# Kernel tuning notes

Hardware: AMD Instinct MI355X
Metric: run time of the kernel (lower is better)

## Reference

```python
import jax, jax.numpy as jnp
import numpy as np

TEMPERATURE = 0.1
NUM_RISK_GROUPS = 4
SIM_WEIGHT = 1.0
CONTRAST_WEIGHT = 0.1
NEG = jnp.float32(-1e9)  # finite stand-in for -inf (grad-safe, exp() == 0 in fp32)


def setup_inputs() -> dict:
    key = jax.random.key(0)
    k1, k2, k3, k4 = jax.random.split(key, 4)
    N, D = 8192, 256
    return {
        "log_risks": jax.random.normal(k1, (N,), dtype=jnp.float32),
        "times": jax.random.uniform(k2, (N,), dtype=jnp.float32),
        "censor": jnp.ones((N,), dtype=jnp.int32),
        "wsi_embeddings": jax.random.normal(k3, (N, D), dtype=jnp.float32),
        "omic_embeddings": jax.random.normal(k4, (N, D), dtype=jnp.float32),
    }


def _cox_loss(log_risks, times, censor):
    lr = jnp.clip(log_risks, -10.0, 10.0)
    order = jnp.argsort(-times)  # descending times
    slr = lr[order]
    sc = censor[order]
    # at-risk sum for index i is sum_{j<=i} exp(slr_j) (arange <= i mask) -> cumsum
    at_risk = jnp.cumsum(jnp.exp(slr))
    li = slr - jnp.log(at_risk + 1e-15)
    mask = (sc == 1)
    cnt = jnp.maximum(jnp.sum(mask), 1)
    return -jnp.sum(jnp.where(mask, li, 0.0)) / cnt


def _similarity_loss(a, b):
    na = jnp.maximum(jnp.linalg.norm(a, axis=1), 1e-8)
    nb = jnp.maximum(jnp.linalg.norm(b, axis=1), 1e-8)
    cos = jnp.clip(jnp.sum(a * b, axis=1) / (na * nb), -1.0, 1.0)
    return jnp.mean(1.0 - cos)


def _contrastive_loss(emb, times):
    # NOTE: assumes censor == 1 for all samples (as in setup_inputs), so the
    # uncensored subset is the whole batch and shapes stay static.
    G = NUM_RISK_GROUPS
    q = jnp.quantile(times, jnp.linspace(0.0, 1.0, G + 1))
    # group = #thresholds q[1..G] that t >= ; max bucket clipped to G-1
    groups = jnp.clip(jnp.sum(times[:, None] >= q[None, 1:], axis=1), 0, G - 1)
    z = emb / jnp.maximum(jnp.linalg.norm(emb, axis=1, keepdims=True), 1e-12)
    sim = (z @ z.T) / TEMPERATURE  # [N, N]
    N = emb.shape[0]
    eye = jnp.eye(N, dtype=bool)
    same = groups[:, None] == groups[None, :]
    pos = same & ~eye
    offdiag = ~eye  # pos | neg == all off-diagonal entries
    lse_pos = jax.nn.logsumexp(jnp.where(pos, sim, NEG), axis=1)
    lse_all = jax.nn.logsumexp(jnp.where(offdiag, sim, NEG), axis=1)
    neg_any = jnp.any(~same & ~eye, axis=1)
    valid = jnp.any(pos, axis=1) & neg_any
    loss = -lse_pos + lse_all
    cnt = jnp.maximum(jnp.sum(valid), 1)
    return jnp.sum(jnp.where(valid, loss, 0.0)) / cnt


def reference(log_risks, times, censor, wsi_embeddings, omic_embeddings):
    cox = _cox_loss(log_risks, times, censor)
    sim = _similarity_loss(wsi_embeddings, omic_embeddings)
    c_wsi = _contrastive_loss(wsi_embeddings, times)
    c_omic = _contrastive_loss(omic_embeddings, times)
    contrast = (c_wsi + c_omic) / 2.0
    return cox + SIM_WEIGHT * sim + CONTRAST_WEIGHT * contrast
```

## Files before the change

kernel.cpp:

```cpp
#include <hip/hip_runtime.h>


#define NN 8192
#define DD 256
#define NSLOT 64

typedef __attribute__((ext_vector_type(4))) float f32x4;
typedef __attribute__((ext_vector_type(4))) int i32x4;
typedef __attribute__((ext_vector_type(2))) long l64x2;

__device__ inline void gl_lds16(const void* g, void* l) {
  __builtin_amdgcn_global_load_lds(
      (const __attribute__((address_space(1))) unsigned int*)g,
      (__attribute__((address_space(3))) unsigned int*)l, 16, 0, 0);
}

__global__ void __launch_bounds__(256) k_rank_atrisk(
    const float* __restrict__ times, const float* __restrict__ lr,
    int* __restrict__ rank, float* __restrict__ at_risk) {
  __shared__ __align__(16) float st[512];
  __shared__ __align__(16) float se[512];
  const int tid = threadIdx.x;
  const int i = blockIdx.x * 256 + tid;
  const int jbase = blockIdx.y * 512;
  for (int p = tid; p < 512; p += 256) {
    float t = times[jbase + p];
    float l = lr[jbase + p];
    l = fminf(fmaxf(l, -10.f), 10.f);
    st[p] = t;
    se[p] = __expf(l);
  }
  __syncthreads();
  const float ti = times[i];
  int rk = 0;
  float ar = 0.f;
  for (int p4 = 0; p4 < 512; p4 += 4) {
    float4 tv = *(const float4*)&st[p4];
    float4 ev = *(const float4*)&se[p4];
    const int j0 = jbase + p4;
#define K1_STEP(c, jo)                                              \
    {                                                               \
      bool c1 = (c < ti) || ((c == ti) && ((j0 + jo) < i));         \
      rk += c1 ? 1 : 0;                                             \
      ar += c1 ? 0.f : ((jo == 0) ? ev.x : (jo == 1) ? ev.y         \
                         : (jo == 2) ? ev.z : ev.w);                \
    }
    K1_STEP(tv.x, 0) K1_STEP(tv.y, 1) K1_STEP(tv.z, 2) K1_STEP(tv.w, 3)
#undef K1_STEP
  }
  atomicAdd(&rank[i], rk);
  atomicAdd(&at_risk[i], ar);
}

__global__ void __launch_bounds__(256) k_rows(
    const float* __restrict__ lr, const int* __restrict__ censor,
    const float* __restrict__ wsi, const float* __restrict__ omic,
    const int* __restrict__ rank, const float* __restrict__ at_risk,
    unsigned char* __restrict__ pw, unsigned char* __restrict__ po,
    float* __restrict__ slots) {
  __shared__ float red[4][3];
  const int tid = threadIdx.x;
  const int lane = tid & 63;
  const int wv = tid >> 6;
  const int i = blockIdx.x * 4 + wv;
  const float4 w = ((const float4*)(wsi + (size_t)i * DD))[lane];
  const float4 o = ((const float4*)(omic + (size_t)i * DD))[lane];
  float nw = w.x * w.x + w.y * w.y + w.z * w.z + w.w * w.w;
  float no = o.x * o.x + o.y * o.y + o.z * o.z + o.w * o.w;
  float dd = w.x * o.x + w.y * o.y + w.z * o.z + w.w * o.w;
  for (int m = 1; m < 64; m <<= 1) {
    nw += __shfl_xor(nw, m);
    no += __shfl_xor(no, m);
    dd += __shfl_xor(dd, m);
  }
  const float nws = sqrtf(nw), nos = sqrtf(no);
  if (lane == 0) {
    float c = dd / (fmaxf(nws, 1e-8f) * fmaxf(nos, 1e-8f));
    c = fminf(fmaxf(c, -1.f), 1.f);
    float l = fminf(fmaxf(lr[i], -10.f), 10.f);
    float li = l - logf(at_risk[i] + 1e-15f);
    bool cen = (censor[i] == 1);
    red[wv][0] = cen ? li : 0.f;
    red[wv][1] = cen ? 1.f : 0.f;
    red[wv][2] = 1.f - c;
  }
  const int r = rank[i];
  const float iw = 1.f / fmaxf(nws, 1e-12f);
  const float io = 1.f / fmaxf(nos, 1e-12f);
  int zw = __builtin_amdgcn_cvt_pk_fp8_f32(w.x * iw, w.y * iw, 0, false);
  zw = __builtin_amdgcn_cvt_pk_fp8_f32(w.z * iw, w.w * iw, zw, true);
  int zo = __builtin_amdgcn_cvt_pk_fp8_f32(o.x * io, o.y * io, 0, false);
  zo = __builtin_amdgcn_cvt_pk_fp8_f32(o.z * io, o.w * io, zo, true);
  const size_t off = ((size_t)((lane >> 4) * 4 + ((lane >> 1) & 3)) * NN + r) * 16
                     + ((lane >> 3) & 1) * 8 + (lane & 1) * 4;
  *(unsigned int*)(pw + off) = (unsigned int)zw;
  *(unsigned int*)(po + off) = (unsigned int)zo;
  __syncthreads();
  if (tid < 3) {
    float v = red[0][tid] + red[1][tid] + red[2][tid] + red[3][tid];
    atomicAdd(&slots[tid * NSLOT + (blockIdx.x & (NSLOT - 1))], v);
  }
}

__global__ void __launch_bounds__(256, 3) k_contrast(
    const unsigned char* __restrict__ pw, const unsigned char* __restrict__ po,
    float* __restrict__ gsum) {
  __shared__ __align__(16) unsigned char sbuf[2][16384];
  const int tid = threadIdx.x;
  const int lane = tid & 63;
  const int wv = tid >> 6;
  const int lo = lane & 15, q = lane >> 4;
  const int cb = blockIdx.x, rb = blockIdx.y, mz = blockIdx.z;
  const unsigned char* __restrict__ pk = (mz == 0) ? pw : po;
  const int rowbase = rb * 256 + wv * 64;
  const int colstart = cb * 512;
  const int g = cb >> 2;

  i32x4 afrag[4][4];
#pragma unroll
  for (int rt = 0; rt < 4; ++rt) {
    const size_t row = rowbase + rt * 16 + lo;
#pragma unroll
    for (int kp = 0; kp < 4; ++kp)
      afrag[rt][kp] = *(const i32x4*)(pk + ((size_t)(kp * 4 + q) * NN + row) * 16);
  }

  const unsigned char* gsrc[4];
#pragma unroll
  for (int p = 0; p < 4; ++p) {
    const int u = (wv * 4 + p) * 64 + lane;
    gsrc[p] = pk + ((size_t)(((u >> 6) & 3) * 4 + ((u >> 4) & 3)) * NN
                    + colstart + (u >> 8) * 16 + (u & 15)) * 16;
  }
  unsigned char* const ldb = &sbuf[0][(size_t)wv * 4096];

#pragma unroll
  for (int p = 0; p < 4; ++p) gl_lds16(gsrc[p], ldb + p * 1024);
  __syncthreads();

  float s[4][4] = {{0.f}};

#pragma unroll 1
  for (int st = 0; st < 8; ++st) {
    if (st < 7) {
      const size_t adv = (size_t)(st + 1) * 1024;
      const size_t bofs = ((st + 1) & 1) ? 16384 : 0;
#pragma unroll
      for (int p = 0; p < 4; ++p) gl_lds16(gsrc[p] + adv, ldb + bofs + p * 1024);
    }
    const unsigned char* buf = &sbuf[st & 1][0];
    const bool diagw = (rowbase == colstart + st * 64);
#pragma unroll
    for (int ct = 0; ct < 4; ++ct) {
      f32x4 acc[4];
#pragma unroll
      for (int rt = 0; rt < 4; ++rt) { f32x4 z = {0.f, 0.f, 0.f, 0.f}; acc[rt] = z; }
#pragma unroll
      for (int kh = 0; kh < 2; ++kh) {
        l64x2 b0 = __builtin_bit_cast(l64x2,
            *(const i32x4*)&buf[(ct * 4 + kh * 2 + 0) * 1024 + lane * 16]);
        l64x2 b1 = __builtin_bit_cast(l64x2,
            *(const i32x4*)&buf[(ct * 4 + kh * 2 + 1) * 1024 + lane * 16]);
#pragma unroll
        for (int rt = 0; rt < 4; ++rt) {
          l64x2 a0 = __builtin_bit_cast(l64x2, afrag[rt][kh * 2 + 0]);
          acc[rt] = __builtin_amdgcn_mfma_f32_16x16x32_fp8_fp8(a0[0], b0[0], acc[rt], 0, 0, 0);
          acc[rt] = __builtin_amdgcn_mfma_f32_16x16x32_fp8_fp8(a0[1], b0[1], acc[rt], 0, 0, 0);
        }
#pragma unroll
        for (int rt = 0; rt < 4; ++rt) {
          l64x2 a1 = __builtin_bit_cast(l64x2, afrag[rt][kh * 2 + 1]);
          acc[rt] = __builtin_amdgcn_mfma_f32_16x16x32_fp8_fp8(a1[0], b1[0], acc[rt], 0, 0, 0);
          acc[rt] = __builtin_amdgcn_mfma_f32_16x16x32_fp8_fp8(a1[1], b1[1], acc[rt], 0, 0, 0);
        }
      }
      if (diagw) {
#pragma unroll
        for (int rt = 0; rt < 4; ++rt)
#pragma unroll
          for (int r = 0; r < 4; ++r) {
            float e = __expf(fmaf(acc[rt][r], 10.f, -10.f));
            if (rt == ct && lo == q * 4 + r) e = 0.f;
            s[rt][r] += e;
          }
      } else {
#pragma unroll
        for (int rt = 0; rt < 4; ++rt)
#pragma unroll
          for (int r = 0; r < 4; ++r)
            s[rt][r] += __expf(fmaf(acc[rt][r], 10.f, -10.f));
      }
    }
    __syncthreads();
  }

#pragma unroll
  for (int rt = 0; rt < 4; ++rt)
#pragma unroll
    for (int r = 0; r < 4; ++r) {
      float v = s[rt][r];
      v += __shfl_xor(v, 1); v += __shfl_xor(v, 2);
      v += __shfl_xor(v, 4); v += __shfl_xor(v, 8);
      if (lo == 0) {
        const int row = rowbase + rt * 16 + q * 4 + r;
        atomicAdd(&gsum[((size_t)mz * NN + row) * 4 + g], v);
      }
    }
}

__global__ void __launch_bounds__(256) k_lse(
    const float* __restrict__ gsum, float* __restrict__ slots) {
  __shared__ float r4[4];
  const int tid = threadIdx.x;
  const int lane = tid & 63, wv = tid >> 6;
  const int idx = blockIdx.x * 256 + tid;
  const float4 v = ((const float4*)gsum)[idx];
  const int row = idx & (NN - 1);
  const int gg = row >> 11;
  const float sg = (gg == 0) ? v.x : (gg == 1) ? v.y : (gg == 2) ? v.z : v.w;
  float loss = logf(v.x + v.y + v.z + v.w) - logf(sg);
  for (int m = 1; m < 64; m <<= 1) loss += __shfl_xor(loss, m);
  if (lane == 0) r4[wv] = loss;
  __syncthreads();
  if (tid == 0)
    atomicAdd(&slots[3 * NSLOT + (blockIdx.x & (NSLOT - 1))],
              r4[0] + r4[1] + r4[2] + r4[3]);
}

__global__ void k_final(const float* __restrict__ slots, float* __restrict__ out) {
  const int lane = threadIdx.x & 63;
  float cox_s = (lane < NSLOT) ? slots[0 * NSLOT + lane] : 0.f;
  float cnt_s = (lane < NSLOT) ? slots[1 * NSLOT + lane] : 0.f;
  float sim_s = (lane < NSLOT) ? slots[2 * NSLOT + lane] : 0.f;
  float con_s = (lane < NSLOT) ? slots[3 * NSLOT + lane] : 0.f;
  for (int m = 1; m < 64; m <<= 1) {
    cox_s += __shfl_xor(cox_s, m);
    cnt_s += __shfl_xor(cnt_s, m);
    sim_s += __shfl_xor(sim_s, m);
    con_s += __shfl_xor(con_s, m);
  }
  if (lane == 0) {
    float cnt = fmaxf(cnt_s, 1.f);
    float cox = -cox_s / cnt;
    float sim = sim_s / (float)NN;
    float contrast = 0.1f * 0.5f * con_s / (float)NN;
    out[0] = cox + sim + contrast;
  }
}

extern "C" void kernel_launch(void* const* d_in, const int* in_sizes, int n_in,
                              void* d_out, int out_size, void* d_ws, size_t ws_size,
                              hipStream_t stream) {
  const float* lr = (const float*)d_in[0];
  const float* times = (const float*)d_in[1];
  const int* censor = (const int*)d_in[2];
  const float* wsi = (const float*)d_in[3];
  const float* omic = (const float*)d_in[4];
  float* out = (float*)d_out;

  char* ws = (char*)d_ws;
  int* rank = (int*)ws;
  float* at_risk = (float*)(ws + 32768);
  float* slots = (float*)(ws + 65536);
  float* gsum = (float*)(ws + 66560);
  unsigned char* pw = (unsigned char*)(ws + 393216);
  unsigned char* po = (unsigned char*)(ws + 393216 + 2097152);

  (void)hipMemsetAsync(d_ws, 0, 328704, stream);
  k_rank_atrisk<<<dim3(32, 16), 256, 0, stream>>>(times, lr, rank, at_risk);
  k_rows<<<2048, 256, 0, stream>>>(lr, censor, wsi, omic, rank, at_risk, pw, po, slots);
  k_contrast<<<dim3(16, 32, 2), 256, 0, stream>>>(pw, po, gsum);
  k_lse<<<64, 256, 0, stream>>>(gsum, slots);
  k_final<<<1, 64, 0, stream>>>(slots, out);
}
```

Measured before the change: 169.7 us.

## Fuse rank/at-risk into row kernel, shrink contrast tiles, merge final reductions

Drops the separate rank/at-risk kernel and the memset. Each wave in k_rows now computes its row's rank and at-risk sum itself by scanning all times, and k_rows also zeroes gsum. k_contrast gives each wave 32 rows instead of 64, which doubles the grid and raises the occupancy hint, and the LSE and final reductions merge into one 1024-thread kernel. This cuts launches and atomics, but every wave now does an O(N) scan, which adds redundant loads and compute, and the single-block finale reduces 16K rows serially per thread.

```diff
diff --git a/kernel.cpp b/kernel.cpp
--- a/kernel.cpp
+++ b/kernel.cpp
@@ -3,7 +3,6 @@
 
 #define NN 8192
 #define DD 256
-#define NSLOT 64
 
 typedef __attribute__((ext_vector_type(4))) float f32x4;
 typedef __attribute__((ext_vector_type(4))) int i32x4;
@@ -15,54 +14,24 @@
       (__attribute__((address_space(3))) unsigned int*)l, 16, 0, 0);
 }
 
-__global__ void __launch_bounds__(256) k_rank_atrisk(
-    const float* __restrict__ times, const float* __restrict__ lr,
-    int* __restrict__ rank, float* __restrict__ at_risk) {
-  __shared__ __align__(16) float st[512];
-  __shared__ __align__(16) float se[512];
-  const int tid = threadIdx.x;
-  const int i = blockIdx.x * 256 + tid;
-  const int jbase = blockIdx.y * 512;
-  for (int p = tid; p < 512; p += 256) {
-    float t = times[jbase + p];
-    float l = lr[jbase + p];
-    l = fminf(fmaxf(l, -10.f), 10.f);
-    st[p] = t;
-    se[p] = __expf(l);
-  }
-  __syncthreads();
-  const float ti = times[i];
-  int rk = 0;
-  float ar = 0.f;
-  for (int p4 = 0; p4 < 512; p4 += 4) {
-    float4 tv = *(const float4*)&st[p4];
-    float4 ev = *(const float4*)&se[p4];
-    const int j0 = jbase + p4;
-#define K1_STEP(c, jo)                                              \
-    {                                                               \
-      bool c1 = (c < ti) || ((c == ti) && ((j0 + jo) < i));         \
-      rk += c1 ? 1 : 0;                                             \
-      ar += c1 ? 0.f : ((jo == 0) ? ev.x : (jo == 1) ? ev.y         \
-                         : (jo == 2) ? ev.z : ev.w);                \
-    }
-    K1_STEP(tv.x, 0) K1_STEP(tv.y, 1) K1_STEP(tv.z, 2) K1_STEP(tv.w, 3)
-#undef K1_STEP
-  }
-  atomicAdd(&rank[i], rk);
-  atomicAdd(&at_risk[i], ar);
-}
-
 __global__ void __launch_bounds__(256) k_rows(
-    const float* __restrict__ lr, const int* __restrict__ censor,
+    const float* __restrict__ lr, const float* __restrict__ times,
+    const int* __restrict__ censor,
     const float* __restrict__ wsi, const float* __restrict__ omic,
-    const int* __restrict__ rank, const float* __restrict__ at_risk,
     unsigned char* __restrict__ pw, unsigned char* __restrict__ po,
-    float* __restrict__ slots) {
+    float* __restrict__ pslots, float* __restrict__ gsum) {
+  __shared__ __align__(16) float st[1024];
+  __shared__ __align__(16) float se[1024];
   __shared__ float red[4][3];
   const int tid = threadIdx.x;
   const int lane = tid & 63;
   const int wv = tid >> 6;
   const int i = blockIdx.x * 4 + wv;
+
+  if (blockIdx.x < 64) {
+    ((f32x4*)gsum)[blockIdx.x * 256 + tid] = (f32x4){0.f, 0.f, 0.f, 0.f};
+  }
+
   const float4 w = ((const float4*)(wsi + (size_t)i * DD))[lane];
   const float4 o = ((const float4*)(omic + (size_t)i * DD))[lane];
   float nw = w.x * w.x + w.y * w.y + w.z * w.z + w.w * w.w;
@@ -74,17 +43,46 @@
     dd += __shfl_xor(dd, m);
   }
   const float nws = sqrtf(nw), nos = sqrtf(no);
+
+  const float ti = times[i];
+  int rk = 0;
+  float ar = 0.f;
+  for (int c = 0; c < 8; ++c) {
+    __syncthreads();
+    for (int p = tid; p < 1024; p += 256) {
+      float t = times[c * 1024 + p];
+      float l = lr[c * 1024 + p];
+      st[p] = t;
+      se[p] = __expf(fminf(fmaxf(l, -10.f), 10.f));
+    }
+    __syncthreads();
+#pragma unroll 4
+    for (int jt = 0; jt < 16; ++jt) {
+      const int p = jt * 64 + lane;
+      const float t = st[p];
+      const float e = se[p];
+      const bool c1 = (t < ti) || ((t == ti) && ((c * 1024 + p) < i));
+      rk += c1 ? 1 : 0;
+      ar += c1 ? 0.f : e;
+    }
+  }
+  for (int m = 1; m < 64; m <<= 1) {
+    rk += __shfl_xor(rk, m);
+    ar += __shfl_xor(ar, m);
+  }
+
   if (lane == 0) {
     float c = dd / (fmaxf(nws, 1e-8f) * fmaxf(nos, 1e-8f));
     c = fminf(fmaxf(c, -1.f), 1.f);
     float l = fminf(fmaxf(lr[i], -10.f), 10.f);
-    float li = l - logf(at_risk[i] + 1e-15f);
+    float li = l - logf(ar + 1e-15f);
     bool cen = (censor[i] == 1);
     red[wv][0] = cen ? li : 0.f;
     red[wv][1] = cen ? 1.f : 0.f;
     red[wv][2] = 1.f - c;
   }
-  const int r = rank[i];
+
+  const int r = rk;
   const float iw = 1.f / fmaxf(nws, 1e-12f);
   const float io = 1.f / fmaxf(nos, 1e-12f);
   int zw = __builtin_amdgcn_cvt_pk_fp8_f32(w.x * iw, w.y * iw, 0, false);
@@ -97,12 +95,12 @@
   *(unsigned int*)(po + off) = (unsigned int)zo;
   __syncthreads();
   if (tid < 3) {
-    float v = red[0][tid] + red[1][tid] + red[2][tid] + red[3][tid];
-    atomicAdd(&slots[tid * NSLOT + (blockIdx.x & (NSLOT - 1))], v);
-  }
-}
-
-__global__ void __launch_bounds__(256, 3) k_contrast(
+    pslots[blockIdx.x * 4 + tid] =
+        red[0][tid] + red[1][tid] + red[2][tid] + red[3][tid];
+  }
+}
+
+__global__ void __launch_bounds__(256, 4) k_contrast(
     const unsigned char* __restrict__ pw, const unsigned char* __restrict__ po,
     float* __restrict__ gsum) {
   __shared__ __align__(16) unsigned char sbuf[2][16384];
@@ -112,13 +110,13 @@
   const int lo = lane & 15, q = lane >> 4;
   const int cb = blockIdx.x, rb = blockIdx.y, mz = blockIdx.z;
   const unsigned char* __restrict__ pk = (mz == 0) ? pw : po;
-  const int rowbase = rb * 256 + wv * 64;
+  const int rowbase = rb * 128 + wv * 32;
   const int colstart = cb * 512;
   const int g = cb >> 2;
 
-  i32x4 afrag[4][4];
-#pragma unroll
-  for (int rt = 0; rt < 4; ++rt) {
+  i32x4 afrag[2][4];
+#pragma unroll
+  for (int rt = 0; rt < 2; ++rt) {
     const size_t row = rowbase + rt * 16 + lo;
 #pragma unroll
     for (int kp = 0; kp < 4; ++kp)
@@ -138,7 +136,8 @@
   for (int p = 0; p < 4; ++p) gl_lds16(gsrc[p], ldb + p * 1024);
   __syncthreads();
 
-  float s[4][4] = {{0.f}};
+  float s[2][4] = {{0.f}};
+  const int dctbase = (wv & 1) * 2;
 
 #pragma unroll 1
   for (int st = 0; st < 8; ++st) {
@@ -149,53 +148,52 @@
       for (int p = 0; p < 4; ++p) gl_lds16(gsrc[p] + adv, ldb + bofs + p * 1024);
     }
     const unsigned char* buf = &sbuf[st & 1][0];
-    const bool diagw = (rowbase == colstart + st * 64);
+    const bool diagw = ((rowbase >> 6) == ((colstart + st * 64) >> 6));
 #pragma unroll
     for (int ct = 0; ct < 4; ++ct) {
-      f32x4 acc[4];
-#pragma unroll
-      for (int rt = 0; rt < 4; ++rt) { f32x4 z = {0.f, 0.f, 0.f, 0.f}; acc[rt] = z; }
+      f32x4 a0 = {0.f, 0.f, 0.f, 0.f}, a1 = {0.f, 0.f, 0.f, 0.f};
 #pragma unroll
       for (int kh = 0; kh < 2; ++kh) {
         l64x2 b0 = __builtin_bit_cast(l64x2,
             *(const i32x4*)&buf[(ct * 4 + kh * 2 + 0) * 1024 + lane * 16]);
         l64x2 b1 = __builtin_bit_cast(l64x2,
             *(const i32x4*)&buf[(ct * 4 + kh * 2 + 1) * 1024 + lane * 16]);
-#pragma unroll
-        for (int rt = 0; rt < 4; ++rt) {
-          l64x2 a0 = __builtin_bit_cast(l64x2, afrag[rt][kh * 2 + 0]);
-          acc[rt] = __builtin_amdgcn_mfma_f32_16x16x32_fp8_fp8(a0[0], b0[0], acc[rt], 0, 0, 0);
-          acc[rt] = __builtin_amdgcn_mfma_f32_16x16x32_fp8_fp8(a0[1], b0[1], acc[rt], 0, 0, 0);
+        l64x2 x0 = __builtin_bit_cast(l64x2, afrag[0][kh * 2 + 0]);
+        l64x2 x1 = __builtin_bit_cast(l64x2, afrag[0][kh * 2 + 1]);
+        l64x2 y0 = __builtin_bit_cast(l64x2, afrag[1][kh * 2 + 0]);
+        l64x2 y1 = __builtin_bit_cast(l64x2, afrag[1][kh * 2 + 1]);
+        a0 = __builtin_amdgcn_mfma_f32_16x16x32_fp8_fp8(x0[0], b0[0], a0, 0, 0, 0);
+        a1 = __builtin_amdgcn_mfma_f32_16x16x32_fp8_fp8(y0[0], b0[0], a1, 0, 0, 0);
+        a0 = __builtin_amdgcn_mfma_f32_16x16x32_fp8_fp8(x0[1], b0[1], a0, 0, 0, 0);
+        a1 = __builtin_amdgcn_mfma_f32_16x16x32_fp8_fp8(y0[1], b0[1], a1, 0, 0, 0);
+        a0 = __builtin_amdgcn_mfma_f32_16x16x32_fp8_fp8(x1[0], b1[0], a0, 0, 0, 0);
+        a1 = __builtin_amdgcn_mfma_f32_16x16x32_fp8_fp8(y1[0], b1[0], a1, 0, 0, 0);
+        a0 = __builtin_amdgcn_mfma_f32_16x16x32_fp8_fp8(x1[1], b1[1], a0, 0, 0, 0);
+        a1 = __builtin_amdgcn_mfma_f32_16x16x32_fp8_fp8(y1[1], b1[1], a1, 0, 0, 0);
+      }
+      if (diagw) {
+#pragma unroll
+        for (int r = 0; r < 4; ++r) {
+          float e0 = __expf(fmaf(a0[r], 10.f, -10.f));
+          float e1 = __expf(fmaf(a1[r], 10.f, -10.f));
+          if (ct == dctbase + 0 && lo == q * 4 + r) e0 = 0.f;
+          if (ct == dctbase + 1 && lo == q * 4 + r) e1 = 0.f;
+          s[0][r] += e0;
+          s[1][r] += e1;
         }
-#pragma unroll
-        for (int rt = 0; rt < 4; ++rt) {
-          l64x2 a1 = __builtin_bit_cast(l64x2, afrag[rt][kh * 2 + 1]);
-          acc[rt] = __builtin_amdgcn_mfma_f32_16x16x32_fp8_fp8(a1[0], b1[0], acc[rt], 0, 0, 0);
-          acc[rt] = __builtin_amdgcn_mfma_f32_16x16x32_fp8_fp8(a1[1], b1[1], acc[rt], 0, 0, 0);
+      } else {
+#pragma unroll
+        for (int r = 0; r < 4; ++r) {
+          s[0][r] += __expf(fmaf(a0[r], 10.f, -10.f));
+          s[1][r] += __expf(fmaf(a1[r], 10.f, -10.f));
         }
       }
-      if (diagw) {
-#pragma unroll
-        for (int rt = 0; rt < 4; ++rt)
-#pragma unroll
-          for (int r = 0; r < 4; ++r) {
-            float e = __expf(fmaf(acc[rt][r], 10.f, -10.f));
-            if (rt == ct && lo == q * 4 + r) e = 0.f;
-            s[rt][r] += e;
-          }
-      } else {
-#pragma unroll
-        for (int rt = 0; rt < 4; ++rt)
-#pragma unroll
-          for (int r = 0; r < 4; ++r)
-            s[rt][r] += __expf(fmaf(acc[rt][r], 10.f, -10.f));
-      }
     }
     __syncthreads();
   }
 
 #pragma unroll
-  for (int rt = 0; rt < 4; ++rt)
+  for (int rt = 0; rt < 2; ++rt)
 #pragma unroll
     for (int r = 0; r < 4; ++r) {
       float v = s[rt][r];
@@ -208,43 +206,41 @@
     }
 }
 
-__global__ void __launch_bounds__(256) k_lse(
-    const float* __restrict__ gsum, float* __restrict__ slots) {
-  __shared__ float r4[4];
+__global__ void __launch_bounds__(1024) k_finale(
+    const float* __restrict__ pslots, const float* __restrict__ gsum,
+    float* __restrict__ out) {
+  __shared__ float rsum[16][4];
   const int tid = threadIdx.x;
   const int lane = tid & 63, wv = tid >> 6;
-  const int idx = blockIdx.x * 256 + tid;
-  const float4 v = ((const float4*)gsum)[idx];
-  const int row = idx & (NN - 1);
-  const int gg = row >> 11;
-  const float sg = (gg == 0) ? v.x : (gg == 1) ? v.y : (gg == 2) ? v.z : v.w;
-  float loss = logf(v.x + v.y + v.z + v.w) - logf(sg);
-  for (int m = 1; m < 64; m <<= 1) loss += __shfl_xor(loss, m);
-  if (lane == 0) r4[wv] = loss;
+  float cox = 0.f, cnt = 0.f, sim = 0.f, con = 0.f;
+  for (int b = tid; b < 2048; b += 1024) {
+    const float4 v = ((const float4*)pslots)[b];
+    cox += v.x; cnt += v.y; sim += v.z;
+  }
+  for (int idx = tid; idx < 2 * NN; idx += 1024) {
+    const float4 v = ((const float4*)gsum)[idx];
+    const int row = idx & (NN - 1);
+    const int gg = row >> 11;
+    const float sg = (gg == 0) ? v.x : (gg == 1) ? v.y : (gg == 2) ? v.z : v.w;
+    con += logf(v.x + v.y + v.z + v.w) - logf(sg);
+  }
+  for (int m = 1; m < 64; m <<= 1) {
+    cox += __shfl_xor(cox, m);
+    cnt += __shfl_xor(cnt, m);
+    sim += __shfl_xor(sim, m);
+    con += __shfl_xor(con, m);
+  }
+  if (lane == 0) {
+    rsum[wv][0] = cox; rsum[wv][1] = cnt; rsum[wv][2] = sim; rsum[wv][3] = con;
+  }
   __syncthreads();
-  if (tid == 0)
-    atomicAdd(&slots[3 * NSLOT + (blockIdx.x & (NSLOT - 1))],
-              r4[0] + r4[1] + r4[2] + r4[3]);
-}
-
-__global__ void k_final(const float* __restrict__ slots, float* __restrict__ out) {
-  const int lane = threadIdx.x & 63;
-  float cox_s = (lane < NSLOT) ? slots[0 * NSLOT + lane] : 0.f;
-  float cnt_s = (lane < NSLOT) ? slots[1 * NSLOT + lane] : 0.f;
-  float sim_s = (lane < NSLOT) ? slots[2 * NSLOT + lane] : 0.f;
-  float con_s = (lane < NSLOT) ? slots[3 * NSLOT + lane] : 0.f;
-  for (int m = 1; m < 64; m <<= 1) {
-    cox_s += __shfl_xor(cox_s, m);
-    cnt_s += __shfl_xor(cnt_s, m);
-    sim_s += __shfl_xor(sim_s, m);
-    con_s += __shfl_xor(con_s, m);
-  }
-  if (lane == 0) {
-    float cnt = fmaxf(cnt_s, 1.f);
-    float cox = -cox_s / cnt;
-    float sim = sim_s / (float)NN;
-    float contrast = 0.1f * 0.5f * con_s / (float)NN;
-    out[0] = cox + sim + contrast;
+  if (tid == 0) {
+    float c0 = 0.f, c1 = 0.f, c2 = 0.f, c3 = 0.f;
+    for (int k = 0; k < 16; ++k) {
+      c0 += rsum[k][0]; c1 += rsum[k][1]; c2 += rsum[k][2]; c3 += rsum[k][3];
+    }
+    out[0] = -c0 / fmaxf(c1, 1.f) + c2 / (float)NN
+             + 0.1f * 0.5f * c3 / (float)NN;
   }
 }
 
@@ -259,17 +255,12 @@
   float* out = (float*)d_out;
 
   char* ws = (char*)d_ws;
-  int* rank = (int*)ws;
-  float* at_risk = (float*)(ws + 32768);
-  float* slots = (float*)(ws + 65536);
-  float* gsum = (float*)(ws + 66560);
-  unsigned char* pw = (unsigned char*)(ws + 393216);
-  unsigned char* po = (unsigned char*)(ws + 393216 + 2097152);
-
-  (void)hipMemsetAsync(d_ws, 0, 328704, stream);
-  k_rank_atrisk<<<dim3(32, 16), 256, 0, stream>>>(times, lr, rank, at_risk);
-  k_rows<<<2048, 256, 0, stream>>>(lr, censor, wsi, omic, rank, at_risk, pw, po, slots);
-  k_contrast<<<dim3(16, 32, 2), 256, 0, stream>>>(pw, po, gsum);
-  k_lse<<<64, 256, 0, stream>>>(gsum, slots);
-  k_final<<<1, 64, 0, stream>>>(slots, out);
-}
+  float* pslots = (float*)ws;
+  float* gsum = (float*)(ws + 32768);
+  unsigned char* pw = (unsigned char*)(ws + 294912);
+  unsigned char* po = (unsigned char*)(ws + 294912 + 2097152);
+
+  k_rows<<<2048, 256, 0, stream>>>(lr, times, censor, wsi, omic, pw, po, pslots, gsum);
+  k_contrast<<<dim3(16, 64, 2), 256, 0, stream>>>(pw, po, gsum);
+  k_finale<<<1, 1024, 0, stream>>>(pslots, gsum, out);
+}
```

Result: faster. 157.0 us (-7.5%).
